# Optimization experiments

Measured on AMD Instinct MI355X. Metric: run time of the kernel, lower is better.

The kernel has to match this reference:

```python
import math
import jax, jax.numpy as jnp
import numpy as np

STREAMS = 4
DIM = 1024
M = 16                      # routing granularity
BUS = STREAMS * DIM         # 4096
C = BUS // M                # 256
SINK_ITERS = 10
SINK_TAU = 0.05
B, L = 4, 2048


def rms_norm(x, gamma):
    # F.normalize(x, dim=-1) * sqrt(dim) * (gamma + 1)
    norm = jnp.sqrt(jnp.sum(x * x, axis=-1, keepdims=True))
    x = x / jnp.maximum(norm, 1e-12)
    return x * jnp.sqrt(jnp.asarray(x.shape[-1], x.dtype)) * (gamma + 1.0)


def sinkhorn_log(logits, num_iters=SINK_ITERS, tau=SINK_TAU):
    n = logits.shape[-1]
    Z = logits / tau
    lm = -math.log(n)
    u = jnp.zeros(Z.shape[:-1], Z.dtype)
    v = jnp.zeros(Z.shape[:-2] + (n,), Z.dtype)
    def body(_, uv):
        u, v = uv
        u = lm - jax.nn.logsumexp(Z + v[..., None, :], axis=-1)
        v = lm - jax.nn.logsumexp(Z + u[..., None], axis=-2)
        return (u, v)
    u, v = jax.lax.fori_loop(0, num_iters, body, (u, v))
    return jnp.exp(Z + u[..., None] + v[..., None, :]) * n


def setup_inputs() -> dict:
    key = jax.random.key(0)
    ks = jax.random.split(key, 8)
    residuals = jax.random.normal(ks[0], (B * STREAMS, L, DIM), jnp.float32)
    branch_output = jax.random.normal(ks[1], (B, L, DIM), jnp.float32)
    gamma = jax.random.normal(ks[2], (BUS,), jnp.float32) * 0.02
    H_res_logits = jnp.full((M, M), -8.0, jnp.float32)
    H_res_logits = H_res_logits.at[jnp.arange(M), jnp.arange(M)].set(0.0)
    phi_res = jax.random.normal(ks[3], (BUS, M * M), jnp.float32) * 0.02
    H_pre_logits = jnp.full((STREAMS,), -8.0, jnp.float32).at[0].set(0.0)
    phi_pre = jax.random.normal(ks[4], (BUS, STREAMS), jnp.float32) * 0.02
    H_post_logits = jnp.zeros((STREAMS,), jnp.float32)
    phi_post = jax.random.normal(ks[5], (BUS, STREAMS), jnp.float32) * 0.02
    a = jnp.asarray(0.01, jnp.float32)
    return dict(residuals=residuals, branch_output=branch_output, gamma=gamma,
                H_res_logits=H_res_logits, phi_res=phi_res, alpha_res=a,
                H_pre_logits=H_pre_logits, phi_pre=phi_pre, alpha_pre=a,
                H_post_logits=H_post_logits, phi_post=phi_post, alpha_post=a)


def reference(residuals, branch_output, gamma, H_res_logits, phi_res, alpha_res,
              H_pre_logits, phi_pre, alpha_pre, H_post_logits, phi_post, alpha_post):
    # (b s) l d -> b l s d
    res = residuals.reshape(B, STREAMS, L, DIM).transpose(0, 2, 1, 3)
    bus = res.reshape(B, L, BUS)
    bus_n = rms_norm(bus, gamma)

    raw = (bus_n @ phi_res).reshape(B, L, M, M)
    S = sinkhorn_log(alpha_res * raw + H_res_logits)
    H_res = S  # no identity mix

    H_pre = jax.nn.softmax(alpha_pre * (bus_n @ phi_pre) + H_pre_logits, axis=-1)
    H_post = jax.nn.softmax(alpha_post * (bus_n @ phi_post) + H_post_logits, axis=-1)

    reshaped = res.reshape(B, L, M, C)
    mixed = jnp.einsum('blst,blsc->bltc', H_res, reshaped).reshape(B, L, STREAMS, DIM)

    branch_input = jnp.einsum('bls,blsd->bld', H_pre, res)

    # depth connection with given branch_output
    branch_to_streams = branch_output[..., None, :] * H_post[..., :, None]
    out = mixed + branch_to_streams            # (B, L, STREAMS, DIM)
    out = out.transpose(0, 2, 1, 3).reshape(B * STREAMS, L, DIM)
    return out, branch_input
```

## Files before the change

### kernel.cpp

```cpp
#include <hip/hip_runtime.h>
#include <hip/hip_bf16.h>
#include <math.h>

#define NSTREAM 4
#define DIM     1024
#define BUSW    4096
#define NTOK    8192
#define NPAD    288
#define KSPLIT  4
#define KCH     1024
#define BM      64
#define BK      32
#define OUT0    ((size_t)16 * 2048 * 1024)

typedef short bf16x8 __attribute__((ext_vector_type(8)));
typedef float f32x4  __attribute__((ext_vector_type(4)));

__device__ __forceinline__ unsigned short f2bf(float f) {
    union { float f; unsigned int u; } x; x.f = f;
    unsigned int r = x.u + 0x7fffu + ((x.u >> 16) & 1u);
    return (unsigned short)(r >> 16);
}
__device__ __forceinline__ unsigned int pack2(float a, float b) {
    return (unsigned int)f2bf(a) | ((unsigned int)f2bf(b) << 16);
}

__device__ __forceinline__ void gload_lds16(const void* g, void* l) {
    __builtin_amdgcn_global_load_lds(
        (const __attribute__((address_space(1))) unsigned int*)g,
        (__attribute__((address_space(3))) unsigned int*)l, 16, 0, 0);
}

__global__ void prep_w_kernel(const float* __restrict__ gamma,
                              const float* __restrict__ phi_res,
                              const float* __restrict__ phi_pre,
                              const float* __restrict__ phi_post,
                              unsigned short* __restrict__ W) {
    int idx = blockIdx.x * 256 + threadIdx.x;
    int n = idx >> 12;
    int k = idx & 4095;
    float v = 0.0f;
    if (n < 256)      v = phi_res[k * 256 + n];
    else if (n < 260) v = phi_pre[k * 4 + (n - 256)];
    else if (n < 264) v = phi_post[k * 4 + (n - 260)];
    v *= (gamma[k] + 1.0f);
    W[idx] = f2bf(v);
}

__launch_bounds__(256, 4)
__global__ void gemm_raw_kernel(const float* __restrict__ residuals,
                                const unsigned short* __restrict__ W,
                                float* __restrict__ raw_part) {
    __shared__ __align__(16) unsigned short Alds[BM * BK];
    __shared__ __align__(16) unsigned short Blds[NPAD * BK];

    const int tid = threadIdx.x;
    const int wid = tid >> 6, lane = tid & 63;
    const int tb = blockIdx.x, kc = blockIdx.y;
    const int row0 = tb * BM;

    f32x4 acc[2][9];
#pragma unroll
    for (int i = 0; i < 2; i++)
#pragma unroll
        for (int j = 0; j < 9; j++) acc[i][j] = (f32x4){0.f, 0.f, 0.f, 0.f};

    const int arow = tid >> 2;
    const int akq  = (tid & 3) * 8;
    const int tok  = row0 + arow;
    const int bidx = tok >> 11, lidx = tok & 2047;
    const float* abase = residuals +
        (((size_t)(bidx * 4 + kc) * 2048 + lidx) * 1024 + akq);
    const char* wbytes = (const char*)(W + (size_t)kc * KCH);

    const int fr = lane & 15, hf = lane >> 4;
    const int wr = (wid >> 1) * 32;
    const int wc = (wid & 1) * 144;

    for (int kt = 0; kt < KCH / BK; kt++) {
#pragma unroll
        for (int i = 0; i < 5; i++) {
            int idx = i * 256 + tid;
            if (idx < (NPAD * BK) / 8) {
                int rn = idx >> 2;
                const void* g = wbytes + (size_t)rn * (BUSW * 2) + kt * (BK * 2)
                                + (idx & 3) * 16;
                gload_lds16(g, (char*)Blds + idx * 16);
            }
        }
        const float* ap = abase + kt * BK;
        float4 f0 = *(const float4*)(ap);
        float4 f1 = *(const float4*)(ap + 4);
        uint4 ua;
        ua.x = pack2(f0.x, f0.y); ua.y = pack2(f0.z, f0.w);
        ua.z = pack2(f1.x, f1.y); ua.w = pack2(f1.z, f1.w);
        *(uint4*)&Alds[arow * BK + akq] = ua;
        __syncthreads();

        bf16x8 afrag[2];
#pragma unroll
        for (int mt = 0; mt < 2; mt++)
            afrag[mt] = *(const bf16x8*)&Alds[(wr + mt * 16 + fr) * BK + hf * 8];
#pragma unroll
        for (int nt = 0; nt < 9; nt++) {
            bf16x8 bfrag = *(const bf16x8*)&Blds[(wc + nt * 16 + fr) * BK + hf * 8];
            acc[0][nt] = __builtin_amdgcn_mfma_f32_16x16x32_bf16(
                afrag[0], bfrag, acc[0][nt], 0, 0, 0);
            acc[1][nt] = __builtin_amdgcn_mfma_f32_16x16x32_bf16(
                afrag[1], bfrag, acc[1][nt], 0, 0, 0);
        }
        __syncthreads();
    }

#pragma unroll
    for (int mt = 0; mt < 2; mt++)
#pragma unroll
        for (int nt = 0; nt < 9; nt++)
#pragma unroll
            for (int r = 0; r < 4; r++) {
                int token = row0 + wr + mt * 16 + hf * 4 + r;
                int col   = wc + nt * 16 + fr;
                raw_part[((size_t)kc * NTOK + token) * NPAD + col] = acc[mt][nt][r];
            }
}

__global__ void fused_tail_kernel(const float* __restrict__ residuals,
                                  const float* __restrict__ branch_output,
                                  const float* __restrict__ H_res_logits,
                                  const float* __restrict__ alpha_res_p,
                                  const float* __restrict__ H_pre_logits,
                                  const float* __restrict__ alpha_pre_p,
                                  const float* __restrict__ H_post_logits,
                                  const float* __restrict__ alpha_post_p,
                                  const float* __restrict__ raw_part,
                                  float* __restrict__ out) {
    const int t = blockIdx.x;
    const int b = t >> 11, l = t & 2047;
    const int tid = threadIdx.x;
    const int wid = tid >> 6, lane = tid & 63;

    __shared__ float Zl[256];
    __shared__ float au[16], bv[16];
    __shared__ float extra[8];
    __shared__ float hpre[4], hpost[4];
    __shared__ float redbuf[4];

    float rsum = 0.f;
#pragma unroll
    for (int kc = 0; kc < 4; kc++)
        rsum += raw_part[((size_t)kc * NTOK + t) * NPAD + tid];
    float esum = 0.f;
    if (tid < 8) {
#pragma unroll
        for (int kc = 0; kc < 4; kc++)
            esum += raw_part[((size_t)kc * NTOK + t) * NPAD + 256 + tid];
    }

    const float* rbase = residuals + ((size_t)b * 4 * 2048 + l) * 1024;
    float busr[16];
    float sumsq = 0.f;
#pragma unroll
    for (int j = 0; j < 16; j++) {
        busr[j] = rbase[(size_t)(j >> 2) * 2048 * 1024 + (j & 3) * 256 + tid];
        sumsq += busr[j] * busr[j];
    }
#pragma unroll
    for (int off = 32; off > 0; off >>= 1) sumsq += __shfl_down(sumsq, off, 64);
    if (lane == 0) redbuf[wid] = sumsq;
    __syncthreads();

    const float ss = redbuf[0] + redbuf[1] + redbuf[2] + redbuf[3];
    const float scale = 64.0f / fmaxf(sqrtf(ss), 1e-12f);

    const float a_res = alpha_res_p[0];
    Zl[tid] = __expf((a_res * scale * rsum + H_res_logits[tid]) * 20.0f);
    if (tid < 8) extra[tid] = esum;

    const float* bo = branch_output + ((size_t)b * 2048 + l) * 1024;
    float bor[4];
#pragma unroll
    for (int j = 0; j < 4; j++) bor[j] = bo[j * 256 + tid];

    __syncthreads();

    if (wid == 0) {
        const float c0 = 1.0f / 16.0f;
        const bool act = lane < 16;
        const int r = lane & 15;
        if (act) bv[r] = 1.0f;
        __builtin_amdgcn_sched_barrier(0);
        float a_own = 0.f;
        for (int it = 0; it < 10; it++) {
            if (act) {
                float s2 = 0.f;
#pragma unroll
                for (int c = 0; c < 16; c++) s2 += Zl[r * 16 + c] * bv[c];
                a_own = c0 / s2;
                au[r] = a_own;
            }
            __builtin_amdgcn_sched_barrier(0);
            if (act) {
                float s2 = 0.f;
#pragma unroll
                for (int rr = 0; rr < 16; rr++) s2 += Zl[rr * 16 + r] * au[rr];
                bv[r] = c0 / s2;
            }
            __builtin_amdgcn_sched_barrier(0);
        }
        if (act) {
#pragma unroll
            for (int c = 0; c < 16; c++)
                Zl[r * 16 + c] = 16.0f * Zl[r * 16 + c] * a_own * bv[c];
        }
    } else if (wid == 1) {
        if (lane < 8) {
            const int s = lane & 3;
            const bool pre = lane < 4;
            const float alpha = pre ? alpha_pre_p[0] : alpha_post_p[0];
            const float logit = pre ? H_pre_logits[s] : H_post_logits[s];
            float pv = alpha * scale * extra[pre ? s : 4 + s] + logit;
            float pm = fmaxf(pv, __shfl_xor(pv, 1, 4));
            pm = fmaxf(pm, __shfl_xor(pm, 2, 4));
            float e = __expf(pv - pm);
            float s2 = e + __shfl_xor(e, 1, 4);
            s2 += __shfl_xor(s2, 2, 4);
            float h = e / s2;
            if (pre) hpre[s] = h; else hpost[s] = h;
        }
    }
    __syncthreads();

#pragma unroll
    for (int tc = 0; tc < 16; tc++) {
        float acc2 = 0.f;
#pragma unroll
        for (int s = 0; s < 16; s++) acc2 += Zl[s * 16 + tc] * busr[s];
        int sout = tc >> 2, d = (tc & 3) * 256 + tid;
        float val = acc2 + bor[tc & 3] * hpost[sout];
        out[((size_t)(b * 4 + sout) * 2048 + l) * 1024 + d] = val;
    }

#pragma unroll
    for (int q = 0; q < 4; q++) {
        float bi = 0.f;
#pragma unroll
        for (int s = 0; s < 4; s++) bi += hpre[s] * busr[s * 4 + q];
        out[OUT0 + ((size_t)b * 2048 + l) * 1024 + q * 256 + tid] = bi;
    }
}

extern "C" void kernel_launch(void* const* d_in, const int* in_sizes, int n_in,
                              void* d_out, int out_size, void* d_ws, size_t ws_size,
                              hipStream_t stream) {
    const float* residuals  = (const float*)d_in[0];
    const float* branch_out = (const float*)d_in[1];
    const float* gamma      = (const float*)d_in[2];
    const float* H_res_log  = (const float*)d_in[3];
    const float* phi_res    = (const float*)d_in[4];
    const float* alpha_res  = (const float*)d_in[5];
    const float* H_pre_log  = (const float*)d_in[6];
    const float* phi_pre    = (const float*)d_in[7];
    const float* alpha_pre  = (const float*)d_in[8];
    const float* H_post_log = (const float*)d_in[9];
    const float* phi_post   = (const float*)d_in[10];
    const float* alpha_post = (const float*)d_in[11];

    unsigned short* W = (unsigned short*)d_ws;
    float* raw_part = (float*)((char*)d_ws + (size_t)NPAD * BUSW * 2);
    float* out = (float*)d_out;

    hipLaunchKernelGGL(prep_w_kernel, dim3(NPAD * BUSW / 256), dim3(256), 0, stream,
                       gamma, phi_res, phi_pre, phi_post, W);
    hipLaunchKernelGGL(gemm_raw_kernel, dim3(NTOK / BM, KSPLIT), dim3(256), 0, stream,
                       residuals, W, raw_part);
    hipLaunchKernelGGL(fused_tail_kernel, dim3(NTOK), dim3(256), 0, stream,
                       residuals, branch_out, H_res_log, alpha_res,
                       H_pre_log, alpha_pre, H_post_log, alpha_post, raw_part, out);
}
```

Before: 383.2 us.

## Restructure GEMM to 2 waves with 64x144 warp tiles and XOR-swizzled LDS

The raw-logit GEMM drops from 4 waves to 2 per block. Each wave now computes all 64 rows by 144 columns, so each B fragment is reused across 4 M tiles instead of 2. LDS tiles for A and B are XOR-swizzled to avoid bank conflicts, and global/LDS address offsets are precomputed outside the k-loop. This increases register pressure from 36 accumulators to 144 floats per lane and leaves fewer waves per block to hide global latency.

Measured after the change: 388.2 us. No clear change (+1.3%).

```diff
diff --git a/kernel.cpp b/kernel.cpp
--- a/kernel.cpp
+++ b/kernel.cpp
@@ -47,7 +47,7 @@
     W[idx] = f2bf(v);
 }
 
-__launch_bounds__(256, 4)
+__launch_bounds__(128, 2)
 __global__ void gemm_raw_kernel(const float* __restrict__ residuals,
                                 const unsigned short* __restrict__ W,
                                 float* __restrict__ raw_part) {
@@ -59,66 +59,91 @@
     const int tb = blockIdx.x, kc = blockIdx.y;
     const int row0 = tb * BM;
 
-    f32x4 acc[2][9];
-#pragma unroll
-    for (int i = 0; i < 2; i++)
+    f32x4 acc[4][9];
+#pragma unroll
+    for (int i = 0; i < 4; i++)
 #pragma unroll
         for (int j = 0; j < 9; j++) acc[i][j] = (f32x4){0.f, 0.f, 0.f, 0.f};
 
-    const int arow = tid >> 2;
-    const int akq  = (tid & 3) * 8;
+    const int arow = tid >> 1;
+    const int akq  = (tid & 1) * 16;
     const int tok  = row0 + arow;
     const int bidx = tok >> 11, lidx = tok & 2047;
     const float* abase = residuals +
         (((size_t)(bidx * 4 + kc) * 2048 + lidx) * 1024 + akq);
+    const int ax = (arow >> 1) & 3;
+    const int j0 = akq >> 3;
+    unsigned short* aw0 = &Alds[(arow * 4 + (j0 ^ ax)) * 8];
+    unsigned short* aw1 = &Alds[(arow * 4 + ((j0 + 1) ^ ax)) * 8];
+
     const char* wbytes = (const char*)(W + (size_t)kc * KCH);
+    const char* bsrc[9];
+    char* bdst[9];
+#pragma unroll
+    for (int i = 0; i < 9; i++) {
+        int idx = i * 128 + tid;
+        int rn = idx >> 2, js = idx & 3;
+        int jg = js ^ ((rn >> 1) & 3);
+        bsrc[i] = wbytes + (size_t)rn * (BUSW * 2) + jg * 16;
+        bdst[i] = (char*)Blds + idx * 16;
+    }
 
     const int fr = lane & 15, hf = lane >> 4;
-    const int wr = (wid >> 1) * 32;
-    const int wc = (wid & 1) * 144;
-
+    const int wc = wid * 144;
+
+    int aoff[4], boff[9];
+#pragma unroll
+    for (int mt = 0; mt < 4; mt++) {
+        int row = mt * 16 + fr;
+        aoff[mt] = (row * 4 + (hf ^ ((row >> 1) & 3))) * 8;
+    }
+#pragma unroll
+    for (int nt = 0; nt < 9; nt++) {
+        int row = wc + nt * 16 + fr;
+        boff[nt] = (row * 4 + (hf ^ ((row >> 1) & 3))) * 8;
+    }
+
+#pragma unroll 1
     for (int kt = 0; kt < KCH / BK; kt++) {
 #pragma unroll
-        for (int i = 0; i < 5; i++) {
-            int idx = i * 256 + tid;
-            if (idx < (NPAD * BK) / 8) {
-                int rn = idx >> 2;
-                const void* g = wbytes + (size_t)rn * (BUSW * 2) + kt * (BK * 2)
-                                + (idx & 3) * 16;
-                gload_lds16(g, (char*)Blds + idx * 16);
-            }
-        }
+        for (int i = 0; i < 9; i++)
+            gload_lds16(bsrc[i] + kt * (BK * 2), bdst[i]);
         const float* ap = abase + kt * BK;
         float4 f0 = *(const float4*)(ap);
         float4 f1 = *(const float4*)(ap + 4);
-        uint4 ua;
-        ua.x = pack2(f0.x, f0.y); ua.y = pack2(f0.z, f0.w);
-        ua.z = pack2(f1.x, f1.y); ua.w = pack2(f1.z, f1.w);
-        *(uint4*)&Alds[arow * BK + akq] = ua;
+        float4 f2 = *(const float4*)(ap + 8);
+        float4 f3 = *(const float4*)(ap + 12);
+        uint4 ua0, ua1;
+        ua0.x = pack2(f0.x, f0.y); ua0.y = pack2(f0.z, f0.w);
+        ua0.z = pack2(f1.x, f1.y); ua0.w = pack2(f1.z, f1.w);
+        ua1.x = pack2(f2.x, f2.y); ua1.y = pack2(f2.z, f2.w);
+        ua1.z = pack2(f3.x, f3.y); ua1.w = pack2(f3.z, f3.w);
+        *(uint4*)aw0 = ua0;
+        *(uint4*)aw1 = ua1;
         __syncthreads();
 
-        bf16x8 afrag[2];
-#pragma unroll
-        for (int mt = 0; mt < 2; mt++)
-            afrag[mt] = *(const bf16x8*)&Alds[(wr + mt * 16 + fr) * BK + hf * 8];
+        bf16x8 afrag[4];
+#pragma unroll
+        for (int mt = 0; mt < 4; mt++)
+            afrag[mt] = *(const bf16x8*)&Alds[aoff[mt]];
 #pragma unroll
         for (int nt = 0; nt < 9; nt++) {
-            bf16x8 bfrag = *(const bf16x8*)&Blds[(wc + nt * 16 + fr) * BK + hf * 8];
-            acc[0][nt] = __builtin_amdgcn_mfma_f32_16x16x32_bf16(
-                afrag[0], bfrag, acc[0][nt], 0, 0, 0);
-            acc[1][nt] = __builtin_amdgcn_mfma_f32_16x16x32_bf16(
-                afrag[1], bfrag, acc[1][nt], 0, 0, 0);
+            bf16x8 bfrag = *(const bf16x8*)&Blds[boff[nt]];
+#pragma unroll
+            for (int mt = 0; mt < 4; mt++)
+                acc[mt][nt] = __builtin_amdgcn_mfma_f32_16x16x32_bf16(
+                    afrag[mt], bfrag, acc[mt][nt], 0, 0, 0);
         }
         __syncthreads();
     }
 
 #pragma unroll
-    for (int mt = 0; mt < 2; mt++)
+    for (int mt = 0; mt < 4; mt++)
 #pragma unroll
         for (int nt = 0; nt < 9; nt++)
 #pragma unroll
             for (int r = 0; r < 4; r++) {
-                int token = row0 + wr + mt * 16 + hf * 4 + r;
+                int token = row0 + mt * 16 + hf * 4 + r;
                 int col   = wc + nt * 16 + fr;
                 raw_part[((size_t)kc * NTOK + token) * NPAD + col] = acc[mt][nt][r];
             }
@@ -271,7 +296,7 @@
 
     hipLaunchKernelGGL(prep_w_kernel, dim3(NPAD * BUSW / 256), dim3(256), 0, stream,
                        gamma, phi_res, phi_pre, phi_post, W);
-    hipLaunchKernelGGL(gemm_raw_kernel, dim3(NTOK / BM, KSPLIT), dim3(256), 0, stream,
+    hipLaunchKernelGGL(gemm_raw_kernel, dim3(NTOK / BM, KSPLIT), dim3(128), 0, stream,
                        residuals, W, raw_part);
     hipLaunchKernelGGL(fused_tail_kernel, dim3(NTOK), dim3(256), 0, stream,
                        residuals, branch_out, H_res_log, alpha_res,
```

## Double-buffer LDS tiles and XOR-swizzle layout in raw GEMM kernel

Applied to the files above, without the earlier changes.

The projection GEMM kernel now keeps two LDS buffers for the A and B tiles. It issues the global loads for the next K tile before running the MFMAs on the current one, which cuts one barrier per iteration. The LDS layout also gets an XOR swizzle on the 16-byte chunks to reduce bank conflicts on the fragment reads. The cost is double the LDS use and occupancy lowered from 4 to 3 waves per SIMD.

Measured after the change: 386.8 us. Within noise of the previous version (+0.9%).

```diff
diff --git a/kernel.cpp b/kernel.cpp
--- a/kernel.cpp
+++ b/kernel.cpp
@@ -47,12 +47,12 @@
     W[idx] = f2bf(v);
 }
 
-__launch_bounds__(256, 4)
+__launch_bounds__(256, 3)
 __global__ void gemm_raw_kernel(const float* __restrict__ residuals,
                                 const unsigned short* __restrict__ W,
                                 float* __restrict__ raw_part) {
-    __shared__ __align__(16) unsigned short Alds[BM * BK];
-    __shared__ __align__(16) unsigned short Blds[NPAD * BK];
+    __shared__ __align__(16) unsigned short Alds[2][BM * BK];
+    __shared__ __align__(16) unsigned short Blds[2][NPAD * BK];
 
     const int tid = threadIdx.x;
     const int wid = tid >> 6, lane = tid & 63;
@@ -66,50 +66,94 @@
         for (int j = 0; j < 9; j++) acc[i][j] = (f32x4){0.f, 0.f, 0.f, 0.f};
 
     const int arow = tid >> 2;
-    const int akq  = (tid & 3) * 8;
+    const int aj   = tid & 3;
     const int tok  = row0 + arow;
     const int bidx = tok >> 11, lidx = tok & 2047;
     const float* abase = residuals +
-        (((size_t)(bidx * 4 + kc) * 2048 + lidx) * 1024 + akq);
+        (((size_t)(bidx * 4 + kc) * 2048 + lidx) * 1024 + aj * 8);
+    const int asl = (arow * 4 + (aj ^ ((arow >> 1) & 3))) * 8;
+
     const char* wbytes = (const char*)(W + (size_t)kc * KCH);
+    const char* bsrc[5];
+    int bdo[5];
+    bool bok[5];
+#pragma unroll
+    for (int i = 0; i < 5; i++) {
+        int idx = i * 256 + tid;
+        bok[i] = idx < (NPAD * BK) / 8;
+        int rn = idx >> 2, js = idx & 3;
+        int jg = js ^ ((rn >> 1) & 3);
+        bsrc[i] = wbytes + (size_t)rn * (BUSW * 2) + jg * 16;
+        bdo[i] = idx * 16;
+    }
 
     const int fr = lane & 15, hf = lane >> 4;
     const int wr = (wid >> 1) * 32;
     const int wc = (wid & 1) * 144;
 
-    for (int kt = 0; kt < KCH / BK; kt++) {
-#pragma unroll
-        for (int i = 0; i < 5; i++) {
-            int idx = i * 256 + tid;
-            if (idx < (NPAD * BK) / 8) {
-                int rn = idx >> 2;
-                const void* g = wbytes + (size_t)rn * (BUSW * 2) + kt * (BK * 2)
-                                + (idx & 3) * 16;
-                gload_lds16(g, (char*)Blds + idx * 16);
-            }
-        }
-        const float* ap = abase + kt * BK;
-        float4 f0 = *(const float4*)(ap);
-        float4 f1 = *(const float4*)(ap + 4);
+    int aoff[2], boff[9];
+#pragma unroll
+    for (int mt = 0; mt < 2; mt++) {
+        int row = wr + mt * 16 + fr;
+        aoff[mt] = (row * 4 + (hf ^ ((row >> 1) & 3))) * 8;
+    }
+#pragma unroll
+    for (int nt = 0; nt < 9; nt++) {
+        int row = wc + nt * 16 + fr;
+        boff[nt] = (row * 4 + (hf ^ ((row >> 1) & 3))) * 8;
+    }
+
+    float4 fa0, fa1;
+
+#pragma unroll
+    for (int i = 0; i < 5; i++)
+        if (bok[i]) gload_lds16(bsrc[i], (char*)Blds[0] + bdo[i]);
+    fa0 = *(const float4*)abase;
+    fa1 = *(const float4*)(abase + 4);
+    {
         uint4 ua;
-        ua.x = pack2(f0.x, f0.y); ua.y = pack2(f0.z, f0.w);
-        ua.z = pack2(f1.x, f1.y); ua.w = pack2(f1.z, f1.w);
-        *(uint4*)&Alds[arow * BK + akq] = ua;
-        __syncthreads();
-
+        ua.x = pack2(fa0.x, fa0.y); ua.y = pack2(fa0.z, fa0.w);
+        ua.z = pack2(fa1.x, fa1.y); ua.w = pack2(fa1.z, fa1.w);
+        *(uint4*)&Alds[0][asl] = ua;
+    }
+    __syncthreads();
+
+    auto step = [&](int kt, int cb, int nb) {
+        if (kt < KCH / BK - 1) {
+#pragma unroll
+            for (int i = 0; i < 5; i++)
+                if (bok[i])
+                    gload_lds16(bsrc[i] + (size_t)(kt + 1) * (BK * 2),
+                                (char*)Blds[nb] + bdo[i]);
+            const float* ap = abase + (kt + 1) * BK;
+            fa0 = *(const float4*)ap;
+            fa1 = *(const float4*)(ap + 4);
+        }
         bf16x8 afrag[2];
 #pragma unroll
         for (int mt = 0; mt < 2; mt++)
-            afrag[mt] = *(const bf16x8*)&Alds[(wr + mt * 16 + fr) * BK + hf * 8];
+            afrag[mt] = *(const bf16x8*)&Alds[cb][aoff[mt]];
 #pragma unroll
         for (int nt = 0; nt < 9; nt++) {
-            bf16x8 bfrag = *(const bf16x8*)&Blds[(wc + nt * 16 + fr) * BK + hf * 8];
+            bf16x8 bfrag = *(const bf16x8*)&Blds[cb][boff[nt]];
             acc[0][nt] = __builtin_amdgcn_mfma_f32_16x16x32_bf16(
                 afrag[0], bfrag, acc[0][nt], 0, 0, 0);
             acc[1][nt] = __builtin_amdgcn_mfma_f32_16x16x32_bf16(
                 afrag[1], bfrag, acc[1][nt], 0, 0, 0);
         }
-        __syncthreads();
+        if (kt < KCH / BK - 1) {
+            uint4 ua;
+            ua.x = pack2(fa0.x, fa0.y); ua.y = pack2(fa0.z, fa0.w);
+            ua.z = pack2(fa1.x, fa1.y); ua.w = pack2(fa1.z, fa1.w);
+            *(uint4*)&Alds[nb][asl] = ua;
+            __syncthreads();
+        }
+    };
+
+#pragma unroll 1
+    for (int kt = 0; kt < KCH / BK; kt += 2) {
+        step(kt,     0, 1);
+        step(kt + 1, 1, 0);
     }
 
 #pragma unroll
```

## Double K-split and XOR-swizzle LDS tiles in the routing GEMM

Applied to the files above, without the earlier changes.

Doubles the GEMM K-split from 4 to 8 chunks of 512, giving twice as many blocks on the GPU. It also applies an XOR swizzle to the A and B tiles in LDS to reduce bank conflicts on the MFMA fragment reads, and precomputes the global and LDS addresses outside the k loop. The cost is twice as many partial-sum rows in raw_part, which the epilogue kernel must now read and add, so that traffic grows.

Result: slower. 393.4 us (+2.6%).

```diff
diff --git a/kernel.cpp b/kernel.cpp
--- a/kernel.cpp
+++ b/kernel.cpp
@@ -7,8 +7,8 @@
 #define BUSW    4096
 #define NTOK    8192
 #define NPAD    288
-#define KSPLIT  4
-#define KCH     1024
+#define KSPLIT  8
+#define KCH     512
 #define BM      64
 #define BK      32
 #define OUT0    ((size_t)16 * 2048 * 1024)
@@ -66,44 +66,66 @@
         for (int j = 0; j < 9; j++) acc[i][j] = (f32x4){0.f, 0.f, 0.f, 0.f};
 
     const int arow = tid >> 2;
-    const int akq  = (tid & 3) * 8;
+    const int aj   = tid & 3;
     const int tok  = row0 + arow;
     const int bidx = tok >> 11, lidx = tok & 2047;
     const float* abase = residuals +
-        (((size_t)(bidx * 4 + kc) * 2048 + lidx) * 1024 + akq);
+        (((size_t)(bidx * 4 + (kc >> 1)) * 2048 + lidx) * 1024
+         + (kc & 1) * KCH + aj * 8);
+    const int asl = (arow * 4 + (aj ^ ((arow >> 1) & 3))) * 8;
+
     const char* wbytes = (const char*)(W + (size_t)kc * KCH);
+    const char* bsrc[5];
+    int bdo[5];
+    bool bok[5];
+#pragma unroll
+    for (int i = 0; i < 5; i++) {
+        int idx = i * 256 + tid;
+        bok[i] = idx < (NPAD * BK) / 8;
+        int rn = idx >> 2, js = idx & 3;
+        int jg = js ^ ((rn >> 1) & 3);
+        bsrc[i] = wbytes + (size_t)rn * (BUSW * 2) + jg * 16;
+        bdo[i] = idx * 16;
+    }
 
     const int fr = lane & 15, hf = lane >> 4;
     const int wr = (wid >> 1) * 32;
     const int wc = (wid & 1) * 144;
 
+    int aoff[2], boff[9];
+#pragma unroll
+    for (int mt = 0; mt < 2; mt++) {
+        int row = wr + mt * 16 + fr;
+        aoff[mt] = (row * 4 + (hf ^ ((row >> 1) & 3))) * 8;
+    }
+#pragma unroll
+    for (int nt = 0; nt < 9; nt++) {
+        int row = wc + nt * 16 + fr;
+        boff[nt] = (row * 4 + (hf ^ ((row >> 1) & 3))) * 8;
+    }
+
+#pragma unroll 1
     for (int kt = 0; kt < KCH / BK; kt++) {
 #pragma unroll
-        for (int i = 0; i < 5; i++) {
-            int idx = i * 256 + tid;
-            if (idx < (NPAD * BK) / 8) {
-                int rn = idx >> 2;
-                const void* g = wbytes + (size_t)rn * (BUSW * 2) + kt * (BK * 2)
-                                + (idx & 3) * 16;
-                gload_lds16(g, (char*)Blds + idx * 16);
-            }
-        }
+        for (int i = 0; i < 5; i++)
+            if (bok[i]) gload_lds16(bsrc[i] + (size_t)kt * (BK * 2),
+                                    (char*)Blds + bdo[i]);
         const float* ap = abase + kt * BK;
         float4 f0 = *(const float4*)(ap);
         float4 f1 = *(const float4*)(ap + 4);
         uint4 ua;
         ua.x = pack2(f0.x, f0.y); ua.y = pack2(f0.z, f0.w);
         ua.z = pack2(f1.x, f1.y); ua.w = pack2(f1.z, f1.w);
-        *(uint4*)&Alds[arow * BK + akq] = ua;
+        *(uint4*)&Alds[asl] = ua;
         __syncthreads();
 
         bf16x8 afrag[2];
 #pragma unroll
         for (int mt = 0; mt < 2; mt++)
-            afrag[mt] = *(const bf16x8*)&Alds[(wr + mt * 16 + fr) * BK + hf * 8];
+            afrag[mt] = *(const bf16x8*)&Alds[aoff[mt]];
 #pragma unroll
         for (int nt = 0; nt < 9; nt++) {
-            bf16x8 bfrag = *(const bf16x8*)&Blds[(wc + nt * 16 + fr) * BK + hf * 8];
+            bf16x8 bfrag = *(const bf16x8*)&Blds[boff[nt]];
             acc[0][nt] = __builtin_amdgcn_mfma_f32_16x16x32_bf16(
                 afrag[0], bfrag, acc[0][nt], 0, 0, 0);
             acc[1][nt] = __builtin_amdgcn_mfma_f32_16x16x32_bf16(
@@ -147,12 +169,12 @@
 
     float rsum = 0.f;
 #pragma unroll
-    for (int kc = 0; kc < 4; kc++)
+    for (int kc = 0; kc < KSPLIT; kc++)
         rsum += raw_part[((size_t)kc * NTOK + t) * NPAD + tid];
     float esum = 0.f;
     if (tid < 8) {
 #pragma unroll
-        for (int kc = 0; kc < 4; kc++)
+        for (int kc = 0; kc < KSPLIT; kc++)
             esum += raw_part[((size_t)kc * NTOK + t) * NPAD + 256 + tid];
     }
 
```
